# Kernel tuning notes

Hardware: AMD Instinct MI355X
Metric: run time of the kernel (lower is better)

Reference implementation:

```python
import jax, jax.numpy as jnp
import numpy as np

BS, C_IN, C_OUT, K, STYLE_DIM, BANK = 8, 64, 64, 3, 512, 4
D = H = W = 32
EPS = 1e-8
STRIDE = 1
PAD = 1


def setup_inputs() -> dict:
    key = jax.random.key(0)
    ks = jax.random.split(key, 7)
    lim_f = 1.0 / np.sqrt(STYLE_DIM)
    return {
        "x": jax.random.normal(ks[0], (BS, C_IN, D, H, W), dtype=jnp.float32),
        "w": jax.random.normal(ks[1], (BS, STYLE_DIM), dtype=jnp.float32),
        "filter_w": jax.random.uniform(ks[2], (BANK, STYLE_DIM), jnp.float32, -lim_f, lim_f),
        "filter_b": jax.random.uniform(ks[3], (BANK,), jnp.float32, -lim_f, lim_f),
        "mod_w": jax.random.uniform(ks[4], (C_IN, STYLE_DIM), jnp.float32, -lim_f, lim_f),
        "mod_b": jax.random.uniform(ks[5], (C_IN,), jnp.float32, -lim_f, lim_f),
        "bank": jax.random.normal(ks[6], (BANK, C_OUT, C_IN, K, K, K), dtype=jnp.float32),
    }


def reference(x, w, filter_w, filter_b, mod_w, mod_b, bank):
    bs, c_in, d, h, ww = x.shape
    # bank selection weights: softmax over bank axis
    fwt = jax.nn.softmax(w @ filter_w.T + filter_b, axis=-1)          # [bs, bank]
    # per-sample weights from bank (bank layout: n, out, in, k, k, k)
    weighted = jnp.einsum('bn,noijkl->boijkl', fwt, bank)             # [bs, out, in, k, k, k]
    # style modulation over input channels
    mod = (w @ mod_w.T + mod_b).reshape(bs, 1, c_in, 1, 1, 1)
    mw = weighted * mod
    # demodulation: normalize each (sample, out-channel) filter
    demod = jax.lax.rsqrt(jnp.sum(mw * mw, axis=(2, 3, 4, 5), keepdims=True) + EPS)
    mw = mw * demod
    # grouped conv with groups = bs
    mw = mw.reshape(bs * C_OUT, c_in, K, K, K)
    xr = x.reshape(1, bs * c_in, d, h, ww)
    out = jax.lax.conv_general_dilated(
        xr, mw,
        window_strides=(STRIDE,) * 3,
        padding=[(PAD, PAD)] * 3,
        dimension_numbers=('NCDHW', 'OIDHW', 'NCDHW'),
        feature_group_count=bs,
    )
    return out.reshape(bs, C_OUT, out.shape[-3], out.shape[-2], out.shape[-1])
```

## Files before the change

kernel.cpp:

```cpp
#include <hip/hip_runtime.h>
#include <math.h>

#define BS 8
#define CIN 64
#define COUT 64
#define SDIM 512
#define NBANK 4
#define DSZ 32
#define SPATIAL (DSZ*DSZ*DSZ)
#define NTAP 27
#define CH 8
#define NCH 8
#define KROW 216
#define NKS 7
#define SLABTEX (1124*33)
#define WINTEX 3301
#define XSTEX 3301
#define ATEX 1728
constexpr float EPS = 1e-8f;

typedef short bf16x8 __attribute__((ext_vector_type(8)));
typedef float f32x4 __attribute__((ext_vector_type(4)));

#define XP_TEXELS (64*SLABTEX)
#define WA_TEXELS (64*ATEX)

__device__ __forceinline__ unsigned pack2(float a, float b) {
    unsigned ua = __float_as_uint(a);
    unsigned ub = __float_as_uint(b);
    ua = (ua + 0x7fffu + ((ua >> 16) & 1u)) >> 16;
    ub = (ub + 0x7fffu + ((ub >> 16) & 1u)) & 0xffff0000u;
    return ua | ub;
}
__device__ __forceinline__ unsigned short bf16r(float f) {
    unsigned u = __float_as_uint(f);
    u = (u + 0x7fffu + ((u >> 16) & 1u)) >> 16;
    return (unsigned short)u;
}

__device__ __forceinline__ void gload_lds16(const int4* g, int4* l) {
    __builtin_amdgcn_global_load_lds(
        (const __attribute__((address_space(1))) unsigned int*)(const void*)g,
        (__attribute__((address_space(3))) unsigned int*)(void*)l, 16, 0, 0);
}

__global__ void prep_style(const float* __restrict__ w,
                           const float* __restrict__ filter_w,
                           const float* __restrict__ filter_b,
                           const float* __restrict__ mod_w,
                           const float* __restrict__ mod_b,
                           float* __restrict__ fwt,
                           float* __restrict__ mod) {
    const int b = blockIdx.x;
    const int t = threadIdx.x;
    const float* wb = w + b * SDIM;
    __shared__ float lg[NBANK];

    if (t < NBANK) {
        float s = filter_b[t];
        const float* fr = filter_w + t * SDIM;
        for (int j = 0; j < SDIM; ++j) s += wb[j] * fr[j];
        lg[t] = s;
    }
    __syncthreads();
    if (t == 0) {
        float m = lg[0];
        for (int n = 1; n < NBANK; ++n) m = fmaxf(m, lg[n]);
        float e[NBANK];
        float s = 0.0f;
        for (int n = 0; n < NBANK; ++n) { e[n] = expf(lg[n] - m); s += e[n]; }
        for (int n = 0; n < NBANK; ++n) fwt[b * NBANK + n] = e[n] / s;
    }
    {
        float s = mod_b[t];
        const float* mr = mod_w + t * SDIM;
        for (int j = 0; j < SDIM; ++j) s += wb[j] * mr[j];
        mod[b * CIN + t] = s;
    }
}

__global__ void prep_weights(const float* __restrict__ bank,
                             const float* __restrict__ fwt,
                             const float* __restrict__ mod,
                             unsigned short* __restrict__ wA) {
    const int oc = blockIdx.x;
    const int b  = blockIdx.y;
    const int ic = threadIdx.x;

    const float f0 = fwt[b * NBANK + 0];
    const float f1 = fwt[b * NBANK + 1];
    const float f2 = fwt[b * NBANK + 2];
    const float f3 = fwt[b * NBANK + 3];
    const float m  = mod[b * CIN + ic];

    const float* b0 = bank + (size_t)((0 * COUT + oc) * CIN + ic) * NTAP;
    const float* b1 = bank + (size_t)((1 * COUT + oc) * CIN + ic) * NTAP;
    const float* b2 = bank + (size_t)((2 * COUT + oc) * CIN + ic) * NTAP;
    const float* b3 = bank + (size_t)((3 * COUT + oc) * CIN + ic) * NTAP;

    float v[NTAP];
    float ss = 0.0f;
#pragma unroll
    for (int k = 0; k < NTAP; ++k) {
        float t = f0 * b0[k] + f1 * b1[k] + f2 * b2[k] + f3 * b3[k];
        t *= m;
        v[k] = t;
        ss += t * t;
    }
#pragma unroll
    for (int off = 32; off >= 1; off >>= 1) ss += __shfl_xor(ss, off, 64);
    const float d = rsqrtf(ss + EPS);

    const int chunk = ic >> 3, icl = ic & 7;
    unsigned short* row = wA + ((size_t)((b * NCH + chunk) * COUT + oc)) * KROW;
#pragma unroll
    for (int k = 0; k < NTAP; ++k) row[k * CH + icl] = bf16r(v[k] * d);
}

__global__ __launch_bounds__(256) void xform(const float* __restrict__ x,
                                             int4* __restrict__ xP) {
    const int zidx = blockIdx.x;
    const int ch   = blockIdx.y;
    const int b    = blockIdx.z;
    int4* slab = xP + (size_t)(b * NCH + ch) * SLABTEX;
    const int t = threadIdx.x;
    const int4 z4 = make_int4(0, 0, 0, 0);

    if (zidx >= 32) {
        int base = (zidx == 32) ? 0 : 1090 * 33;
        for (int p = t; p < 34 * 33; p += 256) slab[base + p] = z4;
        return;
    }
    const float* xc = x + ((size_t)b * CIN + ch * CH) * SPATIAL + zidx * 1024;
    int4* dst = slab + (34 + 33 * zidx) * 33;
    for (int p = t; p < 33 * 33; p += 256) {
        const int r  = p / 33;
        const int cx = p - r * 33;
        int4 v = z4;
        if (r < 32 && cx > 0) {
            const float* s = xc + r * 32 + (cx - 1);
            v.x = (int)pack2(s[0 * SPATIAL], s[1 * SPATIAL]);
            v.y = (int)pack2(s[2 * SPATIAL], s[3 * SPATIAL]);
            v.z = (int)pack2(s[4 * SPATIAL], s[5 * SPATIAL]);
            v.w = (int)pack2(s[6 * SPATIAL], s[7 * SPATIAL]);
        }
        dst[p] = v;
    }
}

__global__ __launch_bounds__(512, 2) void conv3d_mfma(
        const int4* __restrict__ xP,
        const int4* __restrict__ wA,
        float* __restrict__ out) {
    const int bid = blockIdx.x;
    const int b = bid & 7, z = bid >> 3;
    const int t  = threadIdx.x;
    const int ln = t & 15;
    const int hi = (t >> 4) & 3;
    const int wv = t >> 6;

    __shared__ int4 smem[2 * XSTEX + 2 * ATEX + 4];

    int offB[NKS];
#pragma unroll
    for (int ks = 0; ks < NKS; ++ks) {
        int tap = ks * 4 + hi;
        if (tap > 26) tap = 0;
        const int dz = tap / 9, r = tap - dz * 9, dy = r / 3, dx = r - dy * 3;
        offB[ks] = (dz * 1089 + dy * 33 + dx) * 16;
    }
    int baseB[8];
#pragma unroll
    for (int st = 0; st < 8; ++st)
        baseB[st] = ((wv * 4 + (st >> 1)) * 33 + (st & 1) * 16 + ln) * 16;
    const int baseA = ln * 432 + hi * 16;

    const size_t slab0 = (size_t)(b * NCH) * SLABTEX;
    const int win = z * 1089;

    int4 xt, at4;
    auto stage = [&](int c, int buf) {
        const int4* xsrc = xP + slab0 + (size_t)c * SLABTEX + win;
        const int4* asrc = wA + (size_t)(b * NCH + c) * ATEX;
        int4* lx = smem + buf * XSTEX;
        int4* la = smem + 2 * XSTEX + buf * ATEX;
        const int wb = (t & ~63);
#pragma unroll
        for (int i = 0; i < 6; ++i)
            gload_lds16(xsrc + i * 512 + t, lx + i * 512 + wb);
#pragma unroll
        for (int i = 0; i < 3; ++i)
            gload_lds16(asrc + i * 512 + t, la + i * 512 + wb);
        if (t < WINTEX - 3072) xt  = xsrc[3072 + t];
        if (t < ATEX - 1536)   at4 = asrc[1536 + t];
    };
    auto wtails = [&](int buf) {
        if (t < WINTEX - 3072) smem[buf * XSTEX + 3072 + t] = xt;
        if (t < ATEX - 1536)   smem[2 * XSTEX + buf * ATEX + 1536 + t] = at4;
    };

    f32x4 acc[4][8];
#pragma unroll
    for (int i = 0; i < 4; ++i)
#pragma unroll
        for (int j = 0; j < 8; ++j) acc[i][j] = (f32x4){0.f, 0.f, 0.f, 0.f};

    stage(0, 0);
    wtails(0);
    __syncthreads();

    const bf16x8 zv = {0, 0, 0, 0, 0, 0, 0, 0};

    for (int c = 0; c < NCH; ++c) {
        if (c < NCH - 1) stage(c + 1, (c + 1) & 1);

        const char* Xb = (const char*)(smem + (c & 1) * XSTEX);
        const char* Ab = (const char*)(smem + 2 * XSTEX + (c & 1) * ATEX);
#pragma unroll
        for (int ks = 0; ks < NKS; ++ks) {
            bf16x8 a[4];
#pragma unroll
            for (int at = 0; at < 4; ++at) {
                bf16x8 av = *(const bf16x8*)(Ab + at * 6912 + baseA + ks * 64);
                if (ks == NKS - 1) a[at] = (hi == 3) ? zv : av;
                else               a[at] = av;
            }
            bf16x8 bfr[8];
#pragma unroll
            for (int st = 0; st < 8; ++st)
                bfr[st] = *(const bf16x8*)(Xb + baseB[st] + offB[ks]);
#pragma unroll
            for (int at = 0; at < 4; ++at)
#pragma unroll
                for (int st = 0; st < 8; ++st)
                    acc[at][st] = __builtin_amdgcn_mfma_f32_16x16x32_bf16(
                        a[at], bfr[st], acc[at][st], 0, 0, 0);
        }
        if (c < NCH - 1) {
            wtails((c + 1) & 1);
            __syncthreads();
        }
    }

    float* ob = out + (size_t)b * COUT * SPATIAL + (size_t)z * 1024;
#pragma unroll
    for (int at = 0; at < 4; ++at) {
        const int oc = at * 16 + hi * 4;
#pragma unroll
        for (int st = 0; st < 8; ++st) {
            const int sp = (wv * 4 + (st >> 1)) * 32 + (st & 1) * 16 + ln;
#pragma unroll
            for (int r = 0; r < 4; ++r)
                ob[(size_t)(oc + r) * SPATIAL + sp] = acc[at][st][r];
        }
    }
}

extern "C" void kernel_launch(void* const* d_in, const int* in_sizes, int n_in,
                              void* d_out, int out_size, void* d_ws, size_t ws_size,
                              hipStream_t stream) {
    const float* x        = (const float*)d_in[0];
    const float* w        = (const float*)d_in[1];
    const float* filter_w = (const float*)d_in[2];
    const float* filter_b = (const float*)d_in[3];
    const float* mod_w    = (const float*)d_in[4];
    const float* mod_b    = (const float*)d_in[5];
    const float* bank     = (const float*)d_in[6];
    float* out = (float*)d_out;

    int4* xP = (int4*)d_ws;
    int4* wA = xP + XP_TEXELS;
    float* fwt = (float*)(wA + WA_TEXELS);
    float* mod = fwt + BS * NBANK;

    prep_style<<<BS, 64, 0, stream>>>(w, filter_w, filter_b, mod_w, mod_b, fwt, mod);
    prep_weights<<<dim3(COUT, BS), 64, 0, stream>>>(bank, fwt, mod,
                                                    (unsigned short*)wA);
    xform<<<dim3(34, NCH, BS), 256, 0, stream>>>(x, xP);
    conv3d_mfma<<<256, 512, 0, stream>>>(xP, wA, out);
}
```

Baseline: 95.93 us.

## Fuse prep kernels into one launch and restructure conv tiling with register-fed weights

Merges the style, weight-prep and input-transform kernels into a single launch, with per-block softmax recomputation and weights written directly in MFMA fragment order (zero-padded 28th tap). The conv kernel now splits each z-slice into two half-height blocks of 256 threads, stages only the needed input rows into LDS, and streams weight fragments straight from global memory into registers with a two-deep prefetch instead of staging them in LDS. Output stores become nontemporal. This cuts launch overhead and LDS traffic, at the cost of redundant style computation per block and more global weight reads.

```diff
diff --git a/kernel.cpp b/kernel.cpp
--- a/kernel.cpp
+++ b/kernel.cpp
@@ -11,19 +11,17 @@
 #define NTAP 27
 #define CH 8
 #define NCH 8
-#define KROW 216
 #define NKS 7
 #define SLABTEX (1124*33)
-#define WINTEX 3301
-#define XSTEX 3301
-#define ATEX 1728
+#define RUNROWS 19
+#define RUNTEX 640
+#define XWTEX (3*RUNTEX)
+#define A2PERB 14336
+#define XP_TEXELS (64*SLABTEX)
 constexpr float EPS = 1e-8f;
 
 typedef short bf16x8 __attribute__((ext_vector_type(8)));
 typedef float f32x4 __attribute__((ext_vector_type(4)));
-
-#define XP_TEXELS (64*SLABTEX)
-#define WA_TEXELS (64*ATEX)
 
 __device__ __forceinline__ unsigned pack2(float a, float b) {
     unsigned ua = __float_as_uint(a);
@@ -37,129 +35,129 @@
     u = (u + 0x7fffu + ((u >> 16) & 1u)) >> 16;
     return (unsigned short)u;
 }
-
 __device__ __forceinline__ void gload_lds16(const int4* g, int4* l) {
     __builtin_amdgcn_global_load_lds(
         (const __attribute__((address_space(1))) unsigned int*)(const void*)g,
         (__attribute__((address_space(3))) unsigned int*)(void*)l, 16, 0, 0);
 }
 
-__global__ void prep_style(const float* __restrict__ w,
-                           const float* __restrict__ filter_w,
-                           const float* __restrict__ filter_b,
-                           const float* __restrict__ mod_w,
-                           const float* __restrict__ mod_b,
-                           float* __restrict__ fwt,
-                           float* __restrict__ mod) {
-    const int b = blockIdx.x;
-    const int t = threadIdx.x;
-    const float* wb = w + b * SDIM;
-    __shared__ float lg[NBANK];
-
-    if (t < NBANK) {
-        float s = filter_b[t];
-        const float* fr = filter_w + t * SDIM;
-        for (int j = 0; j < SDIM; ++j) s += wb[j] * fr[j];
-        lg[t] = s;
-    }
-    __syncthreads();
-    if (t == 0) {
-        float m = lg[0];
-        for (int n = 1; n < NBANK; ++n) m = fmaxf(m, lg[n]);
-        float e[NBANK];
-        float s = 0.0f;
-        for (int n = 0; n < NBANK; ++n) { e[n] = expf(lg[n] - m); s += e[n]; }
-        for (int n = 0; n < NBANK; ++n) fwt[b * NBANK + n] = e[n] / s;
-    }
-    {
-        float s = mod_b[t];
-        const float* mr = mod_w + t * SDIM;
-        for (int j = 0; j < SDIM; ++j) s += wb[j] * mr[j];
-        mod[b * CIN + t] = s;
-    }
-}
-
-__global__ void prep_weights(const float* __restrict__ bank,
-                             const float* __restrict__ fwt,
-                             const float* __restrict__ mod,
-                             unsigned short* __restrict__ wA) {
-    const int oc = blockIdx.x;
-    const int b  = blockIdx.y;
-    const int ic = threadIdx.x;
-
-    const float f0 = fwt[b * NBANK + 0];
-    const float f1 = fwt[b * NBANK + 1];
-    const float f2 = fwt[b * NBANK + 2];
-    const float f3 = fwt[b * NBANK + 3];
-    const float m  = mod[b * CIN + ic];
-
-    const float* b0 = bank + (size_t)((0 * COUT + oc) * CIN + ic) * NTAP;
-    const float* b1 = bank + (size_t)((1 * COUT + oc) * CIN + ic) * NTAP;
-    const float* b2 = bank + (size_t)((2 * COUT + oc) * CIN + ic) * NTAP;
-    const float* b3 = bank + (size_t)((3 * COUT + oc) * CIN + ic) * NTAP;
-
-    float v[NTAP];
-    float ss = 0.0f;
-#pragma unroll
-    for (int k = 0; k < NTAP; ++k) {
-        float t = f0 * b0[k] + f1 * b1[k] + f2 * b2[k] + f3 * b3[k];
-        t *= m;
-        v[k] = t;
-        ss += t * t;
-    }
-#pragma unroll
-    for (int off = 32; off >= 1; off >>= 1) ss += __shfl_xor(ss, off, 64);
-    const float d = rsqrtf(ss + EPS);
-
-    const int chunk = ic >> 3, icl = ic & 7;
-    unsigned short* row = wA + ((size_t)((b * NCH + chunk) * COUT + oc)) * KROW;
-#pragma unroll
-    for (int k = 0; k < NTAP; ++k) row[k * CH + icl] = bf16r(v[k] * d);
-}
-
-__global__ __launch_bounds__(256) void xform(const float* __restrict__ x,
-                                             int4* __restrict__ xP) {
-    const int zidx = blockIdx.x;
-    const int ch   = blockIdx.y;
-    const int b    = blockIdx.z;
-    int4* slab = xP + (size_t)(b * NCH + ch) * SLABTEX;
-    const int t = threadIdx.x;
-    const int4 z4 = make_int4(0, 0, 0, 0);
-
-    if (zidx >= 32) {
-        int base = (zidx == 32) ? 0 : 1090 * 33;
-        for (int p = t; p < 34 * 33; p += 256) slab[base + p] = z4;
-        return;
-    }
-    const float* xc = x + ((size_t)b * CIN + ch * CH) * SPATIAL + zidx * 1024;
-    int4* dst = slab + (34 + 33 * zidx) * 33;
-    for (int p = t; p < 33 * 33; p += 256) {
-        const int r  = p / 33;
-        const int cx = p - r * 33;
-        int4 v = z4;
-        if (r < 32 && cx > 0) {
-            const float* s = xc + r * 32 + (cx - 1);
-            v.x = (int)pack2(s[0 * SPATIAL], s[1 * SPATIAL]);
-            v.y = (int)pack2(s[2 * SPATIAL], s[3 * SPATIAL]);
-            v.z = (int)pack2(s[4 * SPATIAL], s[5 * SPATIAL]);
-            v.w = (int)pack2(s[6 * SPATIAL], s[7 * SPATIAL]);
-        }
-        dst[p] = v;
-    }
-}
-
-__global__ __launch_bounds__(512, 2) void conv3d_mfma(
+__global__ __launch_bounds__(256) void prep_fused(
+        const float* __restrict__ x,
+        const float* __restrict__ w,
+        const float* __restrict__ filter_w,
+        const float* __restrict__ filter_b,
+        const float* __restrict__ mod_w,
+        const float* __restrict__ mod_b,
+        const float* __restrict__ bank,
+        int4* __restrict__ xP,
+        unsigned short* __restrict__ wA2) {
+    const int gid = blockIdx.x;
+    const int t   = threadIdx.x;
+
+    if (gid < 128) {
+        const int b   = gid >> 4;
+        const int oc  = (gid & 15) * 4 + (t >> 6);
+        const int ic  = t & 63;
+        const float* wb = w + b * SDIM;
+
+        float fw[NBANK];
+#pragma unroll
+        for (int n = 0; n < NBANK; ++n) {
+            float p = 0.0f;
+            const float* fr = filter_w + n * SDIM;
+#pragma unroll
+            for (int k = 0; k < 8; ++k) p += wb[ic + 64 * k] * fr[ic + 64 * k];
+#pragma unroll
+            for (int off = 32; off >= 1; off >>= 1) p += __shfl_xor(p, off, 64);
+            fw[n] = p + filter_b[n];
+        }
+        float mx = fmaxf(fmaxf(fw[0], fw[1]), fmaxf(fw[2], fw[3]));
+        float se = 0.0f;
+#pragma unroll
+        for (int n = 0; n < NBANK; ++n) { fw[n] = expf(fw[n] - mx); se += fw[n]; }
+        const float inv = 1.0f / se;
+        const float f0 = fw[0] * inv, f1 = fw[1] * inv, f2 = fw[2] * inv, f3 = fw[3] * inv;
+
+        float m = mod_b[ic];
+        {
+            const float4* wv4 = (const float4*)wb;
+            const float4* mr4 = (const float4*)(mod_w + ic * SDIM);
+            for (int j = 0; j < SDIM / 4; ++j) {
+                float4 a = wv4[j], c = mr4[j];
+                m += a.x * c.x + a.y * c.y + a.z * c.z + a.w * c.w;
+            }
+        }
+
+        const float* b0 = bank + (size_t)((0 * COUT + oc) * CIN + ic) * NTAP;
+        const float* b1 = bank + (size_t)((1 * COUT + oc) * CIN + ic) * NTAP;
+        const float* b2 = bank + (size_t)((2 * COUT + oc) * CIN + ic) * NTAP;
+        const float* b3 = bank + (size_t)((3 * COUT + oc) * CIN + ic) * NTAP;
+
+        float v[NTAP];
+        float ss = 0.0f;
+#pragma unroll
+        for (int k = 0; k < NTAP; ++k) {
+            float tv = f0 * b0[k] + f1 * b1[k] + f2 * b2[k] + f3 * b3[k];
+            tv *= m;
+            v[k] = tv;
+            ss += tv * tv;
+        }
+#pragma unroll
+        for (int off = 32; off >= 1; off >>= 1) ss += __shfl_xor(ss, off, 64);
+        const float d = rsqrtf(ss + EPS);
+
+        const int c_   = ic >> 3, icl = ic & 7;
+        const int at_  = oc >> 4, ln_ = oc & 15;
+        const size_t tb = (size_t)b * A2PERB + (size_t)at_ * 64 + ln_;
+#pragma unroll
+        for (int k = 0; k < 28; ++k) {
+            const float val = (k < NTAP) ? v[k] * d : 0.0f;
+            const size_t tex = tb + (size_t)(c_ * NKS + (k >> 2)) * 256 + (size_t)(k & 3) * 16;
+            wA2[tex * 8 + icl] = bf16r(val);
+        }
+    } else {
+        const int j2   = gid - 128;
+        const int zidx = j2 % 34;
+        const int ch   = (j2 / 34) & 7;
+        const int b    = j2 / 272;
+        int4* slab = xP + (size_t)(b * NCH + ch) * SLABTEX;
+        const int4 z4 = make_int4(0, 0, 0, 0);
+
+        if (zidx >= 32) {
+            const int base = (zidx == 32) ? 0 : 1090 * 33;
+            for (int p = t; p < 34 * 33; p += 256) slab[base + p] = z4;
+            return;
+        }
+        const float* xc = x + ((size_t)b * CIN + ch * CH) * SPATIAL + zidx * 1024;
+        int4* dst = slab + (34 + 33 * zidx) * 33;
+        for (int p = t; p < 33 * 33; p += 256) {
+            const int r  = p / 33;
+            const int cx = p - r * 33;
+            int4 vv = z4;
+            if (r < 32 && cx > 0) {
+                const float* s = xc + r * 32 + (cx - 1);
+                vv.x = (int)pack2(s[0 * SPATIAL], s[1 * SPATIAL]);
+                vv.y = (int)pack2(s[2 * SPATIAL], s[3 * SPATIAL]);
+                vv.z = (int)pack2(s[4 * SPATIAL], s[5 * SPATIAL]);
+                vv.w = (int)pack2(s[6 * SPATIAL], s[7 * SPATIAL]);
+            }
+            dst[p] = vv;
+        }
+    }
+}
+
+__global__ __launch_bounds__(256, 2) void conv3d_mfma(
         const int4* __restrict__ xP,
-        const int4* __restrict__ wA,
+        const int4* __restrict__ wA2,
         float* __restrict__ out) {
     const int bid = blockIdx.x;
-    const int b = bid & 7, z = bid >> 3;
+    const int b = bid & 7, z = (bid >> 3) & 31, h = bid >> 8;
     const int t  = threadIdx.x;
     const int ln = t & 15;
     const int hi = (t >> 4) & 3;
     const int wv = t >> 6;
 
-    __shared__ int4 smem[2 * XSTEX + 2 * ATEX + 4];
+    __shared__ int4 xs[2 * XWTEX];
 
     int offB[NKS];
 #pragma unroll
@@ -167,36 +165,40 @@
         int tap = ks * 4 + hi;
         if (tap > 26) tap = 0;
         const int dz = tap / 9, r = tap - dz * 9, dy = r / 3, dx = r - dy * 3;
-        offB[ks] = (dz * 1089 + dy * 33 + dx) * 16;
+        offB[ks] = (dz * RUNTEX + dy * 33 + dx) * 16;
     }
     int baseB[8];
 #pragma unroll
     for (int st = 0; st < 8; ++st)
         baseB[st] = ((wv * 4 + (st >> 1)) * 33 + (st & 1) * 16 + ln) * 16;
-    const int baseA = ln * 432 + hi * 16;
-
-    const size_t slab0 = (size_t)(b * NCH) * SLABTEX;
-    const int win = z * 1089;
-
-    int4 xt, at4;
-    auto stage = [&](int c, int buf) {
-        const int4* xsrc = xP + slab0 + (size_t)c * SLABTEX + win;
-        const int4* asrc = wA + (size_t)(b * NCH + c) * ATEX;
-        int4* lx = smem + buf * XSTEX;
-        int4* la = smem + 2 * XSTEX + buf * ATEX;
-        const int wb = (t & ~63);
-#pragma unroll
-        for (int i = 0; i < 6; ++i)
-            gload_lds16(xsrc + i * 512 + t, lx + i * 512 + wb);
-#pragma unroll
-        for (int i = 0; i < 3; ++i)
-            gload_lds16(asrc + i * 512 + t, la + i * 512 + wb);
-        if (t < WINTEX - 3072) xt  = xsrc[3072 + t];
-        if (t < ATEX - 1536)   at4 = asrc[1536 + t];
+
+    const int wrow0 = 33 * z + 16 * h;
+    const int lane  = t & 63;
+
+    auto stageX = [&](int c, int buf) {
+        const int4* src = xP + (size_t)(b * NCH + c) * SLABTEX + (size_t)wrow0 * 33;
+        int4* dst = xs + buf * XWTEX;
+#pragma unroll
+        for (int j = 0; j < 8; ++j) {
+            const int i = wv + 4 * j;
+            if (i < 30) {
+                const int r = (i >= 20) ? 2 : ((i >= 10) ? 1 : 0);
+                const int q = i - r * 10;
+                gload_lds16(src + r * 1089 + q * 64 + lane,
+                            dst + r * RUNTEX + q * 64);
+            }
+        }
     };
-    auto wtails = [&](int buf) {
-        if (t < WINTEX - 3072) smem[buf * XSTEX + 3072 + t] = xt;
-        if (t < ATEX - 1536)   smem[2 * XSTEX + buf * ATEX + 1536 + t] = at4;
+
+    const int4* wab = wA2 + (size_t)b * A2PERB;
+    auto loadA = [&](int kk, bf16x8* dstf) {
+        const int kkc = kk > 55 ? 55 : kk;
+        const int4* p = wab + (size_t)kkc * 256 + lane;
+#pragma unroll
+        for (int at = 0; at < 4; ++at) {
+            const int4 vv = p[at * 64];
+            dstf[at] = *(const bf16x8*)&vv;
+        }
     };
 
     f32x4 acc[4][8];
@@ -205,44 +207,40 @@
 #pragma unroll
         for (int j = 0; j < 8; ++j) acc[i][j] = (f32x4){0.f, 0.f, 0.f, 0.f};
 
-    stage(0, 0);
-    wtails(0);
+    bf16x8 af0[4], af1[4];
+
+    stageX(0, 0);
+    loadA(0, af0);
+    loadA(1, af1);
     __syncthreads();
 
-    const bf16x8 zv = {0, 0, 0, 0, 0, 0, 0, 0};
-
-    for (int c = 0; c < NCH; ++c) {
-        if (c < NCH - 1) stage(c + 1, (c + 1) & 1);
-
-        const char* Xb = (const char*)(smem + (c & 1) * XSTEX);
-        const char* Ab = (const char*)(smem + 2 * XSTEX + (c & 1) * ATEX);
+    auto bodyc = [&](int c, bf16x8 (&S0)[4], bf16x8 (&S1)[4]) {
+        if (c + 1 < NCH) stageX(c + 1, (c + 1) & 1);
+        const char* Xb = (const char*)(xs + (c & 1) * XWTEX);
 #pragma unroll
         for (int ks = 0; ks < NKS; ++ks) {
-            bf16x8 a[4];
-#pragma unroll
-            for (int at = 0; at < 4; ++at) {
-                bf16x8 av = *(const bf16x8*)(Ab + at * 6912 + baseA + ks * 64);
-                if (ks == NKS - 1) a[at] = (hi == 3) ? zv : av;
-                else               a[at] = av;
-            }
-            bf16x8 bfr[8];
+            bf16x8* cur = (ks & 1) ? S1 : S0;
+            bf16x8 bf[8];
 #pragma unroll
             for (int st = 0; st < 8; ++st)
-                bfr[st] = *(const bf16x8*)(Xb + baseB[st] + offB[ks]);
+                bf[st] = *(const bf16x8*)(Xb + baseB[st] + offB[ks]);
 #pragma unroll
             for (int at = 0; at < 4; ++at)
 #pragma unroll
                 for (int st = 0; st < 8; ++st)
                     acc[at][st] = __builtin_amdgcn_mfma_f32_16x16x32_bf16(
-                        a[at], bfr[st], acc[at][st], 0, 0, 0);
-        }
-        if (c < NCH - 1) {
-            wtails((c + 1) & 1);
-            __syncthreads();
-        }
-    }
-
-    float* ob = out + (size_t)b * COUT * SPATIAL + (size_t)z * 1024;
+                        cur[at], bf[st], acc[at][st], 0, 0, 0);
+            loadA(c * NKS + ks + 2, cur);
+        }
+        __syncthreads();
+    };
+
+    for (int cp = 0; cp < 4; ++cp) {
+        bodyc(2 * cp,     af0, af1);
+        bodyc(2 * cp + 1, af1, af0);
+    }
+
+    float* ob = out + (size_t)b * COUT * SPATIAL + (size_t)z * 1024 + h * 512;
 #pragma unroll
     for (int at = 0; at < 4; ++at) {
         const int oc = at * 16 + hi * 4;
@@ -251,7 +249,8 @@
             const int sp = (wv * 4 + (st >> 1)) * 32 + (st & 1) * 16 + ln;
 #pragma unroll
             for (int r = 0; r < 4; ++r)
-                ob[(size_t)(oc + r) * SPATIAL + sp] = acc[at][st][r];
+                __builtin_nontemporal_store(
+                    acc[at][st][r], ob + (size_t)(oc + r) * SPATIAL + sp);
         }
     }
 }
@@ -269,13 +268,9 @@
     float* out = (float*)d_out;
 
     int4* xP = (int4*)d_ws;
-    int4* wA = xP + XP_TEXELS;
-    float* fwt = (float*)(wA + WA_TEXELS);
-    float* mod = fwt + BS * NBANK;
-
-    prep_style<<<BS, 64, 0, stream>>>(w, filter_w, filter_b, mod_w, mod_b, fwt, mod);
-    prep_weights<<<dim3(COUT, BS), 64, 0, stream>>>(bank, fwt, mod,
-                                                    (unsigned short*)wA);
-    xform<<<dim3(34, NCH, BS), 256, 0, stream>>>(x, xP);
-    conv3d_mfma<<<256, 512, 0, stream>>>(xP, wA, out);
-}
+    unsigned short* wA2 = (unsigned short*)(xP + XP_TEXELS);
+
+    prep_fused<<<128 + 34 * 8 * 8, 256, 0, stream>>>(
+        x, w, filter_w, filter_b, mod_w, mod_b, bank, xP, wA2);
+    conv3d_mfma<<<512, 256, 0, stream>>>(xP, (const int4*)wA2, out);
+}
```

Result: slower. 128.8 us (+34.2%).
